# Kernel tuning notes

Hardware: AMD Instinct MI355X
Metric: run time of the kernel (lower is better)

## Reference

```python
import jax, jax.numpy as jnp
import numpy as np

HIDDEN = 64

def setup_inputs() -> dict:
    key = jax.random.key(0)
    ks = jax.random.split(key, 6)
    inp = {
        "input_a": jax.random.normal(ks[0], (16, 6209, 256), dtype=jnp.float32),
        "input_b": jax.random.normal(ks[1], (16, 256, 256), dtype=jnp.float32),
        # Linear weights stored as [in, out]; xavier-ish scale
        "Wa": jax.random.normal(ks[2], (256, HIDDEN), dtype=jnp.float32) * (2.0 / (256 + HIDDEN)) ** 0.5,
        "ba": jnp.zeros((HIDDEN,), dtype=jnp.float32),
        "Wb": jax.random.normal(ks[3], (256, HIDDEN), dtype=jnp.float32) * (2.0 / (256 + HIDDEN)) ** 0.5,
        "bb": jnp.zeros((HIDDEN,), dtype=jnp.float32),
        "Wc": jax.random.normal(ks[4], (HIDDEN, 256), dtype=jnp.float32) * (2.0 / (HIDDEN + 256)) ** 0.5,
        "bc": jnp.zeros((256,), dtype=jnp.float32),
    }
    return inp

def reference(input_a, input_b, Wa, ba, Wb, bb, Wc, bc):
    # mapped_a: [b, dima, h], mapped_b: [b, dimb, h]
    mapped_a = jnp.einsum("bif,fh->bih", input_a, Wa) + ba
    mapped_b = jnp.einsum("bjf,fh->bjh", input_b, Wb) + bb
    # NOTE: original divides by scale = hidden**-0.5, i.e. multiplies by sqrt(hidden)
    scores = jnp.einsum("bih,bjh->bij", mapped_a, mapped_b) * jnp.sqrt(jnp.float32(HIDDEN))
    attn = jax.nn.softmax(scores, axis=-1)  # dropout is identity in eval
    out = jnp.einsum("bij,bjh->bih", attn, mapped_b)
    out = jnp.einsum("bih,hf->bif", out, Wc) + bc
    return out
```

## Files before the change

### kernel.cpp

```cpp
#include <hip/hip_runtime.h>

typedef float f32x4 __attribute__((ext_vector_type(4)));
typedef short s16x8 __attribute__((ext_vector_type(8)));

#define MFMA16(a, b, c) __builtin_amdgcn_mfma_f32_16x16x32_bf16((a), (b), (c), 0, 0, 0)

#define B_ 16
#define M_ 6209
#define F_ 256
#define NT_ 392

static __device__ __forceinline__ unsigned short f2bf(float x) {
    unsigned u = __builtin_bit_cast(unsigned, x);
    unsigned r = u + 0x7fffu + ((u >> 16) & 1u);
    return (unsigned short)(r >> 16);
}
static __device__ __forceinline__ float bf2f(unsigned short h) {
    unsigned u = ((unsigned)h) << 16;
    return __builtin_bit_cast(float, u);
}
static __device__ __forceinline__ void split_bf(float x, unsigned short& hi, unsigned short& lo) {
    hi = f2bf(x);
    lo = f2bf(x - bf2f(hi));
}
static __device__ __forceinline__ unsigned cvtpk_bf16(float a, float b) {
    unsigned r;
    asm("v_cvt_pk_bf16_f32 %0, %1, %2" : "=v"(r) : "v"(a), "v"(b));
    return r;
}

#define SW64(row, k)  ((row) * 64 + ((k) ^ (((row) & 7) << 3)))
#define SW256(row, k) ((row) * 256 + ((k) ^ (((row) & 7) << 3)))

__global__ __launch_bounds__(256) void k_pack(
    const float* __restrict__ Wa, const float* __restrict__ Wc,
    unsigned short* __restrict__ waf_hi, unsigned short* __restrict__ waf_lo,
    unsigned short* __restrict__ wcf) {
    const int idx = blockIdx.x * 256 + threadIdx.x;
    if (idx < 16384) {
        int i = idx;
        int jj = i & 7, lane = (i >> 3) & 63, nf = (i >> 9) & 3, ks = i >> 11;
        int g = lane >> 4, c = lane & 15;
        int f = ks * 32 + g * 8 + jj, h = nf * 16 + c;
        unsigned short hi, lo; split_bf(Wa[f * 64 + h], hi, lo);
        waf_hi[i] = hi; waf_lo[i] = lo;
    } else {
        int i = idx - 16384;
        int jj = i & 7, lane = (i >> 3) & 63, nf = (i >> 9) & 15, ks = i >> 13;
        int g = lane >> 4, c = lane & 15;
        int h = ks * 32 + g * 8 + jj, f = nf * 16 + c;
        wcf[i] = f2bf(Wc[h * 256 + f]);
    }
}

__global__ __launch_bounds__(256, 3) void k_work(
    const float* __restrict__ A, const float* __restrict__ ba,
    const unsigned short* __restrict__ waf_hi, const unsigned short* __restrict__ waf_lo,
    const float* __restrict__ inB, const float* __restrict__ Wb, const float* __restrict__ bb,
    unsigned short* __restrict__ mbb_hi, unsigned short* __restrict__ mbb_lo,
    unsigned short* __restrict__ mbp,
    unsigned short* __restrict__ mafh, unsigned short* __restrict__ mafl) {
    __shared__ __align__(16) unsigned short maH[4][1024];
    __shared__ __align__(16) unsigned short maL[4][1024];
    const int blk = blockIdx.x;
    const int w = threadIdx.x >> 6, lane = threadIdx.x & 63;
    if (blk < 784) {
        const int b = blk / 49, bx = blk % 49;
        const int g = lane >> 4, c = lane & 15;
        const int t0 = (bx * 4 + w) * 2;

        f32x4 accA[2][4];
        #pragma unroll
        for (int i = 0; i < 2; ++i)
            #pragma unroll
            for (int nf = 0; nf < 4; ++nf) { float v = ba[nf * 16 + c]; accA[i][nf] = (f32x4){v, v, v, v}; }
        const float* ab[2];
        #pragma unroll
        for (int i = 0; i < 2; ++i) {
            int arow = (t0 + i) * 16 + c; if (arow > M_ - 1) arow = M_ - 1;
            ab[i] = A + ((size_t)b * M_ + arow) * F_;
        }
        #pragma unroll
        for (int ks = 0; ks < 8; ++ks) {
            s16x8 ah[2], al[2];
            #pragma unroll
            for (int i = 0; i < 2; ++i) {
                const f32x4 a0 = *(const f32x4*)(ab[i] + ks * 32 + g * 8);
                const f32x4 a1 = *(const f32x4*)(ab[i] + ks * 32 + g * 8 + 4);
                #pragma unroll
                for (int j = 0; j < 4; ++j) {
                    unsigned short hi, lo;
                    split_bf(a0[j], hi, lo); ah[i][j] = (short)hi; al[i][j] = (short)lo;
                    split_bf(a1[j], hi, lo); ah[i][4 + j] = (short)hi; al[i][4 + j] = (short)lo;
                }
            }
            #pragma unroll
            for (int nf = 0; nf < 4; ++nf) {
                const int off = ((ks * 4 + nf) * 64 + lane) << 3;
                const s16x8 bh = *(const s16x8*)(waf_hi + off);
                const s16x8 bl = *(const s16x8*)(waf_lo + off);
                #pragma unroll
                for (int i = 0; i < 2; ++i) {
                    accA[i][nf] = MFMA16(ah[i], bh, accA[i][nf]);
                    accA[i][nf] = MFMA16(ah[i], bl, accA[i][nf]);
                    accA[i][nf] = MFMA16(al[i], bh, accA[i][nf]);
                }
            }
        }
        #pragma unroll
        for (int i = 0; i < 2; ++i) {
            #pragma unroll
            for (int nf = 0; nf < 4; ++nf)
                #pragma unroll
                for (int r = 0; r < 4; ++r) {
                    unsigned short hi, lo; split_bf(accA[i][nf][r], hi, lo);
                    const int idx = SW64(g * 4 + r, nf * 16 + c);
                    maH[w][idx] = hi; maL[w][idx] = lo;
                }
            #pragma unroll
            for (int ks = 0; ks < 2; ++ks) {
                const s16x8 fh = *(const s16x8*)&maH[w][SW64(c, ks * 32 + g * 8)];
                const s16x8 fl = *(const s16x8*)&maL[w][SW64(c, ks * 32 + g * 8)];
                const size_t off = (((size_t)(b * NT_ + t0 + i) * 2 + ks) * 64 + lane) << 3;
                *(s16x8*)(mafh + off) = fh;
                *(s16x8*)(mafl + off) = fl;
            }
        }
    } else {
        const int idx = blk - 784;
        const int b = idx >> 6;
        const int j = (idx & 63) * 4 + w;
        const int h = lane;
        const float* src = inB + ((size_t)(b * 256 + j)) * 256;
        float s = bb[h];
        #pragma unroll 4
        for (int f4 = 0; f4 < 64; ++f4) {
            const f32x4 v = *(const f32x4*)(src + f4 * 4);
            s = fmaf(v[0], Wb[(f4 * 4 + 0) * 64 + h], s);
            s = fmaf(v[1], Wb[(f4 * 4 + 1) * 64 + h], s);
            s = fmaf(v[2], Wb[(f4 * 4 + 2) * 64 + h], s);
            s = fmaf(v[3], Wb[(f4 * 4 + 3) * 64 + h], s);
        }
        unsigned short hi, lo; split_bf(s, hi, lo);
        const int i1 = (b << 14) | ((h >> 5) << 13) | ((j >> 4) << 9)
                     | (((h >> 3) & 3) << 7) | ((j & 15) << 3) | (h & 7);
        mbb_hi[i1] = hi;
        mbb_lo[i1] = lo;
        const int i2 = (b << 14) | ((j >> 5) << 11) | ((h >> 4) << 9)
                     | (((j >> 3) & 3) << 7) | ((h & 15) << 3) | (j & 7);
        mbp[i2] = hi;
    }
}

__global__ __launch_bounds__(256, 4) void k_attn2(
    const unsigned short* __restrict__ mafh, const unsigned short* __restrict__ mafl,
    const unsigned short* __restrict__ mbb_hi, const unsigned short* __restrict__ mbb_lo,
    const unsigned short* __restrict__ mbp, const unsigned short* __restrict__ wcf,
    const float* __restrict__ bc, float* __restrict__ out) {
    __shared__ __align__(16) unsigned short pSh[2][16 * 256];
    __shared__ __align__(16) unsigned short o1S[2][16 * 64];
    __shared__ float pmaxS[2][4][16];
    __shared__ float psumS[2][4][16];

    const int t0 = blockIdx.x * 2, b = blockIdx.y;
    const int w = threadIdx.x >> 6, lane = threadIdx.x & 63;
    const int g = lane >> 4, c = lane & 15;
    const float SC = 11.541560327f;

    s16x8 bh[2][2], bl[2][2];
    #pragma unroll
    for (int i = 0; i < 2; ++i)
        #pragma unroll
        for (int ks = 0; ks < 2; ++ks) {
            const size_t off = (((size_t)(b * NT_ + t0 + i) * 2 + ks) * 64 + lane) << 3;
            bh[i][ks] = *(const s16x8*)(mafh + off);
            bl[i][ks] = *(const s16x8*)(mafl + off);
        }

    f32x4 accST[2][4];
    #pragma unroll
    for (int i = 0; i < 2; ++i)
        #pragma unroll
        for (int jtl = 0; jtl < 4; ++jtl) accST[i][jtl] = (f32x4){0.f, 0.f, 0.f, 0.f};
    #pragma unroll
    for (int jtl = 0; jtl < 4; ++jtl) {
        const int jt = w * 4 + jtl;
        const size_t off0 = ((((size_t)b * 2 + 0) * 16 + jt) * 64 + lane) << 3;
        const size_t off1 = ((((size_t)b * 2 + 1) * 16 + jt) * 64 + lane) << 3;
        const s16x8 ah0 = *(const s16x8*)(mbb_hi + off0);
        const s16x8 al0 = *(const s16x8*)(mbb_lo + off0);
        const s16x8 ah1 = *(const s16x8*)(mbb_hi + off1);
        const s16x8 al1 = *(const s16x8*)(mbb_lo + off1);
        #pragma unroll
        for (int i = 0; i < 2; ++i) {
            f32x4 acc = accST[i][jtl];
            acc = MFMA16(ah0, bh[i][0], acc);
            acc = MFMA16(ah1, bh[i][1], acc);
            acc = MFMA16(ah0, bl[i][0], acc);
            acc = MFMA16(ah1, bl[i][1], acc);
            acc = MFMA16(al0, bh[i][0], acc);
            acc = MFMA16(al1, bh[i][1], acc);
            accST[i][jtl] = acc;
        }
    }

    #pragma unroll
    for (int i = 0; i < 2; ++i) {
        float m = accST[i][0][0];
        #pragma unroll
        for (int jtl = 0; jtl < 4; ++jtl) {
            m = fmaxf(m, accST[i][jtl][0]); m = fmaxf(m, accST[i][jtl][1]);
            m = fmaxf(m, accST[i][jtl][2]); m = fmaxf(m, accST[i][jtl][3]);
        }
        m = fmaxf(m, __shfl_xor(m, 16));
        m = fmaxf(m, __shfl_xor(m, 32));
        if (lane < 16) pmaxS[i][w][lane] = m;
    }
    __syncthreads();

    #pragma unroll
    for (int i = 0; i < 2; ++i) {
        const float mg = fmaxf(fmaxf(pmaxS[i][0][c], pmaxS[i][1][c]),
                               fmaxf(pmaxS[i][2][c], pmaxS[i][3][c]));
        float s = 0.f;
        #pragma unroll
        for (int jtl = 0; jtl < 4; ++jtl) {
            f32x4 p;
            #pragma unroll
            for (int r = 0; r < 4; ++r) {
                p[r] = __builtin_amdgcn_exp2f((accST[i][jtl][r] - mg) * SC);
                s += p[r];
            }
            const unsigned w0 = cvtpk_bf16(p[0], p[1]);
            const unsigned w1 = cvtpk_bf16(p[2], p[3]);
            const unsigned long long wv = (unsigned long long)w0 | ((unsigned long long)w1 << 32);
            *(unsigned long long*)&pSh[i][SW256(c, (w * 4 + jtl) * 16 + g * 4)] = wv;
        }
        s += __shfl_xor(s, 16);
        s += __shfl_xor(s, 32);
        if (lane < 16) psumS[i][w][lane] = s;
    }
    __syncthreads();

    f32x4 acc1[2] = {(f32x4){0.f, 0.f, 0.f, 0.f}, (f32x4){0.f, 0.f, 0.f, 0.f}};
    #pragma unroll
    for (int ks = 0; ks < 8; ++ks) {
        const size_t off = ((((size_t)b * 8 + ks) * 4 + w) * 64 + lane) << 3;
        const s16x8 av = *(const s16x8*)(mbp + off);
        #pragma unroll
        for (int i = 0; i < 2; ++i) {
            const s16x8 pf = *(const s16x8*)&pSh[i][SW256(c, ks * 32 + g * 8)];
            acc1[i] = MFMA16(av, pf, acc1[i]);
        }
    }
    #pragma unroll
    for (int i = 0; i < 2; ++i) {
        const float rinv = 1.f / (psumS[i][0][c] + psumS[i][1][c] + psumS[i][2][c] + psumS[i][3][c]);
        const unsigned w0 = cvtpk_bf16(acc1[i][0] * rinv, acc1[i][1] * rinv);
        const unsigned w1 = cvtpk_bf16(acc1[i][2] * rinv, acc1[i][3] * rinv);
        const unsigned long long wv = (unsigned long long)w0 | ((unsigned long long)w1 << 32);
        *(unsigned long long*)&o1S[i][SW64(c, w * 16 + g * 4)] = wv;
    }
    __syncthreads();

    s16x8 af[2][2];
    #pragma unroll
    for (int i = 0; i < 2; ++i)
        #pragma unroll
        for (int ks = 0; ks < 2; ++ks)
            af[i][ks] = *(const s16x8*)&o1S[i][SW64(c, ks * 32 + g * 8)];
    #pragma unroll
    for (int ftl = 0; ftl < 4; ++ftl) {
        const int ft = w * 4 + ftl;
        const float bv = bc[ft * 16 + c];
        const s16x8 wb0 = *(const s16x8*)(wcf + (((0 * 16 + ft) * 64 + lane) << 3));
        const s16x8 wb1 = *(const s16x8*)(wcf + (((1 * 16 + ft) * 64 + lane) << 3));
        #pragma unroll
        for (int i = 0; i < 2; ++i) {
            f32x4 acc = (f32x4){bv, bv, bv, bv};
            acc = MFMA16(af[i][0], wb0, acc);
            acc = MFMA16(af[i][1], wb1, acc);
            #pragma unroll
            for (int r = 0; r < 4; ++r) {
                const int q = (t0 + i) * 16 + g * 4 + r;
                if (q < M_) out[((size_t)b * M_ + q) * F_ + ft * 16 + c] = acc[r];
            }
        }
    }
}

extern "C" void kernel_launch(void* const* d_in, const int* in_sizes, int n_in,
                              void* d_out, int out_size, void* d_ws, size_t ws_size,
                              hipStream_t stream) {
    (void)in_sizes; (void)n_in; (void)out_size; (void)ws_size;
    const float* inA = (const float*)d_in[0];
    const float* inB = (const float*)d_in[1];
    const float* Wa  = (const float*)d_in[2];
    const float* ba  = (const float*)d_in[3];
    const float* Wb  = (const float*)d_in[4];
    const float* bb  = (const float*)d_in[5];
    const float* Wc  = (const float*)d_in[6];
    const float* bc  = (const float*)d_in[7];
    float* out = (float*)d_out;

    char* ws = (char*)d_ws;
    unsigned short* waf_hi = (unsigned short*)ws;
    unsigned short* waf_lo = (unsigned short*)(ws + 32768);
    unsigned short* wcf    = (unsigned short*)(ws + 65536);
    unsigned short* mbb_hi = (unsigned short*)(ws + 98304);
    unsigned short* mbb_lo = (unsigned short*)(ws + 622592);
    unsigned short* mbp    = (unsigned short*)(ws + 1146880);
    unsigned short* mafh   = (unsigned short*)(ws + 1671168);
    unsigned short* mafl   = (unsigned short*)(ws + 14516224);

    hipLaunchKernelGGL(k_pack, dim3(128), dim3(256), 0, stream,
                       Wa, Wc, waf_hi, waf_lo, wcf);
    hipLaunchKernelGGL(k_work, dim3(784 + 1024), dim3(256), 0, stream,
                       inA, ba, waf_hi, waf_lo, inB, Wb, bb,
                       mbb_hi, mbb_lo, mbp, mafh, mafl);
    hipLaunchKernelGGL(k_attn2, dim3(195, B_), dim3(256), 0, stream,
                       mafh, mafl, mbb_hi, mbb_lo, mbp, wcf, bc, out);
}
```

Measured before the change: 82.21 us.

## Stage packed Wa in shared memory and halve per-wave row tiles in projection

The A-projection path now has each wave handle one 16-row tile instead of two, which doubles the number of blocks. Each block stages the full packed Wa hi/lo fragments (64 KB) into LDS once instead of every wave reading them from global memory, and all A-row loads are issued up front before the staging. The LDS buffer is reused for the output swizzle after a barrier. The B-projection path splits its serial FMA chain into four independent accumulators to expose ILP. In exchange, occupancy drops to 2 blocks per CU because of the larger LDS footprint, and every block repeats the weight staging.

```diff
diff --git a/kernel.cpp b/kernel.cpp
--- a/kernel.cpp
+++ b/kernel.cpp
@@ -53,94 +53,96 @@
     }
 }
 
-__global__ __launch_bounds__(256, 3) void k_work(
+__global__ __launch_bounds__(256, 2) void k_work(
     const float* __restrict__ A, const float* __restrict__ ba,
     const unsigned short* __restrict__ waf_hi, const unsigned short* __restrict__ waf_lo,
     const float* __restrict__ inB, const float* __restrict__ Wb, const float* __restrict__ bb,
     unsigned short* __restrict__ mbb_hi, unsigned short* __restrict__ mbb_lo,
     unsigned short* __restrict__ mbp,
     unsigned short* __restrict__ mafh, unsigned short* __restrict__ mafl) {
-    __shared__ __align__(16) unsigned short maH[4][1024];
-    __shared__ __align__(16) unsigned short maL[4][1024];
+    __shared__ __align__(16) unsigned short wafS[32768];
     const int blk = blockIdx.x;
     const int w = threadIdx.x >> 6, lane = threadIdx.x & 63;
-    if (blk < 784) {
-        const int b = blk / 49, bx = blk % 49;
+    if (blk < 1568) {
+        const int b = blk / 98, bx = blk % 98;
         const int g = lane >> 4, c = lane & 15;
-        const int t0 = (bx * 4 + w) * 2;
-
-        f32x4 accA[2][4];
-        #pragma unroll
-        for (int i = 0; i < 2; ++i)
-            #pragma unroll
-            for (int nf = 0; nf < 4; ++nf) { float v = ba[nf * 16 + c]; accA[i][nf] = (f32x4){v, v, v, v}; }
-        const float* ab[2];
-        #pragma unroll
-        for (int i = 0; i < 2; ++i) {
-            int arow = (t0 + i) * 16 + c; if (arow > M_ - 1) arow = M_ - 1;
-            ab[i] = A + ((size_t)b * M_ + arow) * F_;
-        }
+        const int t = bx * 4 + w;
+
+        int arow = t * 16 + c; if (arow > M_ - 1) arow = M_ - 1;
+        const float* abase = A + ((size_t)b * M_ + arow) * F_;
+        f32x4 ar0[8], ar1[8];
         #pragma unroll
         for (int ks = 0; ks < 8; ++ks) {
-            s16x8 ah[2], al[2];
-            #pragma unroll
-            for (int i = 0; i < 2; ++i) {
-                const f32x4 a0 = *(const f32x4*)(ab[i] + ks * 32 + g * 8);
-                const f32x4 a1 = *(const f32x4*)(ab[i] + ks * 32 + g * 8 + 4);
-                #pragma unroll
-                for (int j = 0; j < 4; ++j) {
-                    unsigned short hi, lo;
-                    split_bf(a0[j], hi, lo); ah[i][j] = (short)hi; al[i][j] = (short)lo;
-                    split_bf(a1[j], hi, lo); ah[i][4 + j] = (short)hi; al[i][4 + j] = (short)lo;
-                }
+            ar0[ks] = *(const f32x4*)(abase + ks * 32 + g * 8);
+            ar1[ks] = *(const f32x4*)(abase + ks * 32 + g * 8 + 4);
+        }
+
+        #pragma unroll
+        for (int i = 0; i < 8; ++i) {
+            const int o = (i * 256 + threadIdx.x) * 8;
+            *(s16x8*)&wafS[o] = *(const s16x8*)(waf_hi + o);
+            *(s16x8*)&wafS[16384 + o] = *(const s16x8*)(waf_lo + o);
+        }
+        __syncthreads();
+
+        f32x4 accA[4];
+        #pragma unroll
+        for (int nf = 0; nf < 4; ++nf) { float v = ba[nf * 16 + c]; accA[nf] = (f32x4){v, v, v, v}; }
+        #pragma unroll
+        for (int ks = 0; ks < 8; ++ks) {
+            s16x8 ah, al;
+            #pragma unroll
+            for (int j = 0; j < 4; ++j) {
+                unsigned short hi, lo;
+                split_bf(ar0[ks][j], hi, lo); ah[j] = (short)hi; al[j] = (short)lo;
+                split_bf(ar1[ks][j], hi, lo); ah[4 + j] = (short)hi; al[4 + j] = (short)lo;
             }
             #pragma unroll
             for (int nf = 0; nf < 4; ++nf) {
-                const int off = ((ks * 4 + nf) * 64 + lane) << 3;
-                const s16x8 bh = *(const s16x8*)(waf_hi + off);
-                const s16x8 bl = *(const s16x8*)(waf_lo + off);
-                #pragma unroll
-                for (int i = 0; i < 2; ++i) {
-                    accA[i][nf] = MFMA16(ah[i], bh, accA[i][nf]);
-                    accA[i][nf] = MFMA16(ah[i], bl, accA[i][nf]);
-                    accA[i][nf] = MFMA16(al[i], bh, accA[i][nf]);
-                }
-            }
-        }
-        #pragma unroll
-        for (int i = 0; i < 2; ++i) {
-            #pragma unroll
-            for (int nf = 0; nf < 4; ++nf)
-                #pragma unroll
-                for (int r = 0; r < 4; ++r) {
-                    unsigned short hi, lo; split_bf(accA[i][nf][r], hi, lo);
-                    const int idx = SW64(g * 4 + r, nf * 16 + c);
-                    maH[w][idx] = hi; maL[w][idx] = lo;
-                }
-            #pragma unroll
-            for (int ks = 0; ks < 2; ++ks) {
-                const s16x8 fh = *(const s16x8*)&maH[w][SW64(c, ks * 32 + g * 8)];
-                const s16x8 fl = *(const s16x8*)&maL[w][SW64(c, ks * 32 + g * 8)];
-                const size_t off = (((size_t)(b * NT_ + t0 + i) * 2 + ks) * 64 + lane) << 3;
-                *(s16x8*)(mafh + off) = fh;
-                *(s16x8*)(mafl + off) = fl;
-            }
+                const int fo = ((ks * 4 + nf) * 64 + lane) * 8;
+                const s16x8 bh = *(const s16x8*)&wafS[fo];
+                const s16x8 bl = *(const s16x8*)&wafS[16384 + fo];
+                accA[nf] = MFMA16(ah, bh, accA[nf]);
+                accA[nf] = MFMA16(ah, bl, accA[nf]);
+                accA[nf] = MFMA16(al, bh, accA[nf]);
+            }
+        }
+        __syncthreads();
+
+        unsigned short* mH = wafS + w * 2048;
+        unsigned short* mL = mH + 1024;
+        #pragma unroll
+        for (int nf = 0; nf < 4; ++nf)
+            #pragma unroll
+            for (int r = 0; r < 4; ++r) {
+                unsigned short hi, lo; split_bf(accA[nf][r], hi, lo);
+                const int idx = SW64(g * 4 + r, nf * 16 + c);
+                mH[idx] = hi; mL[idx] = lo;
+            }
+        #pragma unroll
+        for (int ks = 0; ks < 2; ++ks) {
+            const s16x8 fh = *(const s16x8*)&mH[SW64(c, ks * 32 + g * 8)];
+            const s16x8 fl = *(const s16x8*)&mL[SW64(c, ks * 32 + g * 8)];
+            const size_t off = (((size_t)(b * NT_ + t) * 2 + ks) * 64 + lane) << 3;
+            *(s16x8*)(mafh + off) = fh;
+            *(s16x8*)(mafl + off) = fl;
         }
     } else {
-        const int idx = blk - 784;
+        const int idx = blk - 1568;
         const int b = idx >> 6;
         const int j = (idx & 63) * 4 + w;
         const int h = lane;
         const float* src = inB + ((size_t)(b * 256 + j)) * 256;
-        float s = bb[h];
+        float s0 = bb[h], s1 = 0.f, s2 = 0.f, s3 = 0.f;
         #pragma unroll 4
         for (int f4 = 0; f4 < 64; ++f4) {
             const f32x4 v = *(const f32x4*)(src + f4 * 4);
-            s = fmaf(v[0], Wb[(f4 * 4 + 0) * 64 + h], s);
-            s = fmaf(v[1], Wb[(f4 * 4 + 1) * 64 + h], s);
-            s = fmaf(v[2], Wb[(f4 * 4 + 2) * 64 + h], s);
-            s = fmaf(v[3], Wb[(f4 * 4 + 3) * 64 + h], s);
-        }
+            s0 = fmaf(v[0], Wb[(f4 * 4 + 0) * 64 + h], s0);
+            s1 = fmaf(v[1], Wb[(f4 * 4 + 1) * 64 + h], s1);
+            s2 = fmaf(v[2], Wb[(f4 * 4 + 2) * 64 + h], s2);
+            s3 = fmaf(v[3], Wb[(f4 * 4 + 3) * 64 + h], s3);
+        }
+        const float s = (s0 + s1) + (s2 + s3);
         unsigned short hi, lo; split_bf(s, hi, lo);
         const int i1 = (b << 14) | ((h >> 5) << 13) | ((j >> 4) << 9)
                      | (((h >> 3) & 3) << 7) | ((j & 15) << 3) | (h & 7);
@@ -315,7 +317,7 @@
 
     hipLaunchKernelGGL(k_pack, dim3(128), dim3(256), 0, stream,
                        Wa, Wc, waf_hi, waf_lo, wcf);
-    hipLaunchKernelGGL(k_work, dim3(784 + 1024), dim3(256), 0, stream,
+    hipLaunchKernelGGL(k_work, dim3(1568 + 1024), dim3(256), 0, stream,
                        inA, ba, waf_hi, waf_lo, inB, Wb, bb,
                        mbb_hi, mbb_lo, mbp, mafh, mafl);
     hipLaunchKernelGGL(k_attn2, dim3(195, B_), dim3(256), 0, stream,
```

New measurement: 83.17 us. No clear change (+1.2%).
